# Kernel optimization log

Hardware: AMD Instinct MI355X
Metric: run time of the kernel (lower is better)

## Reference

```python
import jax, jax.numpy as jnp
import numpy as np

N, E, G = 200000, 800000, 8192
IN, H, D, EXTRA = 128, 4, 64, 16


def setup_inputs() -> dict:
    key = jax.random.key(0)
    ks = jax.random.split(key, 24)
    inp = {
        'feats_node': jax.random.normal(ks[0], (N, IN), jnp.float32),
        'feats_graph': jax.random.normal(ks[1], (G, EXTRA), jnp.float32),
        'src': jax.random.randint(ks[2], (E,), 0, N, jnp.int32),
        'dst': jax.random.randint(ks[3], (E,), 0, N, jnp.int32),
        'graph_ids': jnp.sort(jax.random.randint(ks[4], (N,), 0, G, jnp.int32)),
        # GAT layer 1: fc [H*D, IN], attn [H, D], bias zeros (DGL default)
        'fc1_w': 0.5 * jax.random.normal(ks[5], (H * D, IN), jnp.float32),
        'attn_l1': 0.5 * jax.random.normal(ks[6], (H, D), jnp.float32),
        'attn_r1': 0.5 * jax.random.normal(ks[7], (H, D), jnp.float32),
        'bias1': jnp.zeros((H * D,), jnp.float32),
        # GAT layer 2
        'fc2_w': 0.5 * jax.random.normal(ks[8], (H * D, H * D), jnp.float32),
        'attn_l2': 0.5 * jax.random.normal(ks[9], (H, D), jnp.float32),
        'attn_r2': 0.5 * jax.random.normal(ks[10], (H, D), jnp.float32),
        'bias2': jnp.zeros((H * D,), jnp.float32),
        # GAT layer 3: 1 head
        'fc3_w': 0.5 * jax.random.normal(ks[11], (D, H * D), jnp.float32),
        'attn_l3': 0.5 * jax.random.normal(ks[12], (1, D), jnp.float32),
        'attn_r3': 0.5 * jax.random.normal(ks[13], (1, D), jnp.float32),
        'bias3': jnp.zeros((D,), jnp.float32),
        # readout score
        'score_w': 0.5 * jax.random.normal(ks[14], (1, D), jnp.float32),
        'score_b': jnp.zeros((1,), jnp.float32),
        # MLP: [D+EXTRA -> 2D -> D -> 1]
        'mlp_w1': 0.5 * jax.random.normal(ks[15], (2 * D, D + EXTRA), jnp.float32),
        'mlp_b1': jnp.zeros((2 * D,), jnp.float32),
        'mlp_w2': 0.5 * jax.random.normal(ks[16], (D, 2 * D), jnp.float32),
        'mlp_b2': jnp.zeros((D,), jnp.float32),
        'mlp_w3': 0.5 * jax.random.normal(ks[17], (1, D), jnp.float32),
        'mlp_b3': jnp.zeros((1,), jnp.float32),
    }
    return inp


def gat_conv(x, src, dst, fc_w, attn_l, attn_r, bias, n_heads, out_dim):
    # DGL GATConv: proj -> edge leaky_relu attention -> per-dst softmax -> aggregate
    n = x.shape[0]
    feat = (x @ fc_w.T).reshape(n, n_heads, out_dim)          # [N,H,D]
    el = jnp.einsum('nhd,hd->nh', feat, attn_l)               # [N,H]
    er = jnp.einsum('nhd,hd->nh', feat, attn_r)
    e = jax.nn.leaky_relu(el[src] + er[dst], 0.2)             # [E,H]
    m = jax.ops.segment_max(e, dst, num_segments=n)           # per-dst max
    m = jax.lax.stop_gradient(jnp.where(jnp.isfinite(m), m, 0.0))
    a = jnp.exp(e - m[dst])                                   # [E,H]
    denom = jax.ops.segment_sum(a, dst, num_segments=n)       # [N,H]
    alpha = a / jnp.where(denom[dst] == 0, 1.0, denom[dst])
    out = jax.ops.segment_sum(alpha[:, :, None] * feat[src], dst, num_segments=n)
    return out + bias.reshape(1, n_heads, out_dim)            # [N,H,D]


def reference(feats_node, feats_graph, src, dst, graph_ids,
              fc1_w, attn_l1, attn_r1, bias1,
              fc2_w, attn_l2, attn_r2, bias2,
              fc3_w, attn_l3, attn_r3, bias3,
              score_w, score_b,
              mlp_w1, mlp_b1, mlp_w2, mlp_b2, mlp_w3, mlp_b3):
    n = feats_node.shape[0]
    g = feats_graph.shape[0]
    x = jax.nn.selu(gat_conv(feats_node, src, dst, fc1_w, attn_l1, attn_r1, bias1, H, D)).reshape(n, H * D)
    x = jax.nn.selu(gat_conv(x, src, dst, fc2_w, attn_l2, attn_r2, bias2, H, D)).reshape(n, H * D)
    x = jax.nn.selu(gat_conv(x, src, dst, fc3_w, attn_l3, attn_r3, bias3, 1, D)).reshape(n, D)
    # weighted-average readout: sum(w*x)/sum(w) per graph
    w = jax.nn.sigmoid(x @ score_w.T + score_b)               # [N,1]
    num = jax.ops.segment_sum(w * x, graph_ids, num_segments=g)
    den = jax.ops.segment_sum(w, graph_ids, num_segments=g)
    emb = num / jnp.where(den == 0, 1.0, den)                 # [G,D]
    z = jnp.concatenate([emb, feats_graph], axis=1)           # [G,D+EXTRA]
    h = jax.nn.selu(z @ mlp_w1.T + mlp_b1)
    h = jax.nn.selu(h @ mlp_w2.T + mlp_b2)
    return h @ mlp_w3.T + mlp_b3                              # [G,1]
```

## Files before the change

kernel.cpp:

```cpp
#include <hip/hip_runtime.h>
#include <math.h>

#define N_NODES 200000
#define N_EDGES 800000
#define N_GRAPHS 8192
#define B1 16
#define B2G 16
#define EC2 128

typedef unsigned short ushort_t;

__device__ __forceinline__ float selu_f(float x){
  const float alpha = 1.6732632423543772f;
  const float lam   = 1.0507009873554805f;
  return x > 0.f ? lam * x : lam * alpha * (expf(x) - 1.f);
}

__global__ void zero_i32(int* p, int n){
  int i = blockIdx.x * 256 + threadIdx.x;
  if (i < n) p[i] = 0;
}

__global__ void deg_kernel(const int* __restrict__ dst, int* __restrict__ deg, int E){
  int e = blockIdx.x * 256 + threadIdx.x;
  if (e < E) atomicAdd(&deg[dst[e]], 1);
}

__global__ void scan1(const int* __restrict__ deg, int* __restrict__ rp, int* __restrict__ bs, int n){
  __shared__ int sh[256];
  int t = threadIdx.x;
  int base = blockIdx.x * 1024;
  int v[4]; int s = 0;
  #pragma unroll
  for (int i = 0; i < 4; i++){
    int idx = base + t * 4 + i;
    v[i] = (idx < n) ? deg[idx] : 0;
    s += v[i];
  }
  sh[t] = s; __syncthreads();
  for (int off = 1; off < 256; off <<= 1){
    int x = (t >= off) ? sh[t - off] : 0;
    __syncthreads();
    sh[t] += x;
    __syncthreads();
  }
  int run = (t == 0) ? 0 : sh[t - 1];
  #pragma unroll
  for (int i = 0; i < 4; i++){
    int idx = base + t * 4 + i;
    if (idx < n) rp[idx] = run;
    run += v[i];
  }
  if (t == 255) bs[blockIdx.x] = sh[255];
}

__global__ void scan2(int* bs, int nb){
  __shared__ int sh[256];
  int t = threadIdx.x;
  sh[t] = (t < nb) ? bs[t] : 0; __syncthreads();
  for (int off = 1; off < 256; off <<= 1){
    int x = (t >= off) ? sh[t - off] : 0;
    __syncthreads();
    sh[t] += x;
    __syncthreads();
  }
  int excl = (t == 0) ? 0 : sh[t - 1];
  if (t < nb) bs[t] = excl;
}

__global__ void scan3(int* rp, const int* __restrict__ bs, int n, int total){
  int i = blockIdx.x * 256 + threadIdx.x;
  if (i < n) rp[i] += bs[i >> 10];
  if (i == 0) rp[n] = total;
}

__global__ void fill_csr(const int* __restrict__ src, const int* __restrict__ dst,
                         const int* __restrict__ rp, int* __restrict__ fil,
                         int* __restrict__ csr, int E){
  int e = blockIdx.x * 256 + threadIdx.x;
  if (e < E){
    int d = dst[e];
    int p = atomicAdd(&fil[d], 1);
    csr[rp[d] + p] = src[e];
  }
}

__global__ void wt_kernel(const float* __restrict__ W1, const float* __restrict__ W2,
                          float* __restrict__ W1t, float* __restrict__ W2t){
  int i = blockIdx.x * 256 + threadIdx.x;
  if (i < 32768){
    int k = i >> 8, m = i & 255;
    W1t[i] = W1[(size_t)m * 128 + k];
  } else if (i < 32768 + 65536){
    int j = i - 32768;
    int k = j >> 8, m = j & 255;
    W2t[j] = W2[(size_t)m * 256 + k];
  }
}

__global__ void compute_v(const float* __restrict__ W1, const float* __restrict__ al1, const float* __restrict__ ar1,
                          const float* __restrict__ W2, const float* __restrict__ al2, const float* __restrict__ ar2,
                          const float* __restrict__ W3, const float* __restrict__ al3, const float* __restrict__ ar3,
                          float* __restrict__ V1L, float* __restrict__ V1R,
                          float* __restrict__ V2L, float* __restrict__ V2R,
                          float* __restrict__ V3L, float* __restrict__ V3R){
  int i = blockIdx.x * 256 + threadIdx.x;
  if (i < 512){
    int h = i >> 7, k = i & 127;
    float sl = 0.f, sr = 0.f;
    for (int dd = 0; dd < 64; dd++){
      float w = W1[(size_t)(h * 64 + dd) * 128 + k];
      sl += al1[h * 64 + dd] * w;
      sr += ar1[h * 64 + dd] * w;
    }
    V1L[i] = sl; V1R[i] = sr;
  } else if (i < 1536){
    int j = i - 512;
    int h = j >> 8, k = j & 255;
    float sl = 0.f, sr = 0.f;
    for (int dd = 0; dd < 64; dd++){
      float w = W2[(size_t)(h * 64 + dd) * 256 + k];
      sl += al2[h * 64 + dd] * w;
      sr += ar2[h * 64 + dd] * w;
    }
    V2L[j] = sl; V2R[j] = sr;
  } else if (i < 1792){
    int k = i - 1536;
    float sl = 0.f, sr = 0.f;
    for (int dd = 0; dd < 64; dd++){
      float w = W3[(size_t)dd * 256 + k];
      sl += al3[dd] * w;
      sr += ar3[dd] * w;
    }
    V3L[k] = sl; V3R[k] = sr;
  }
}

__global__ __launch_bounds__(256) void el_er1(const float* __restrict__ x0,
                                              const float* __restrict__ V1L, const float* __restrict__ V1R,
                                              float* __restrict__ el1, float* __restrict__ er1, int n){
  __shared__ float vl[512], vr[512];
  int t = threadIdx.x;
  for (int i = t; i < 512; i += 256){ vl[i] = V1L[i]; vr[i] = V1R[i]; }
  __syncthreads();
  int node = blockIdx.x * 4 + (t >> 6);
  int l = t & 63;
  if (node >= n) return;
  float xa = x0[(size_t)node * 128 + l];
  float xb = x0[(size_t)node * 128 + 64 + l];
  #pragma unroll
  for (int h = 0; h < 4; h++){
    float pl = xa * vl[h * 128 + l] + xb * vl[h * 128 + 64 + l];
    float pr = xa * vr[h * 128 + l] + xb * vr[h * 128 + 64 + l];
    #pragma unroll
    for (int off = 32; off; off >>= 1){ pl += __shfl_xor(pl, off); pr += __shfl_xor(pr, off); }
    if (l == 0){ el1[(size_t)node * 4 + h] = pl; er1[(size_t)node * 4 + h] = pr; }
  }
}

__global__ __launch_bounds__(256) void alpha_h4(const float* __restrict__ el, const float* __restrict__ er,
                                                const int* __restrict__ rp, const int* __restrict__ csr,
                                                float* __restrict__ a, int n){
  int node = blockIdx.x * 256 + threadIdx.x;
  if (node >= n) return;
  int s0 = rp[node], s1 = rp[node + 1];
  if (s0 >= s1) return;
  float4 erv = *reinterpret_cast<const float4*>(er + (size_t)node * 4);
  float m0 = -1e30f, m1 = -1e30f, m2 = -1e30f, m3 = -1e30f;
  for (int i = s0; i < s1; i++){
    float4 e = *reinterpret_cast<const float4*>(el + (size_t)csr[i] * 4);
    float e0 = e.x + erv.x; e0 = e0 > 0.f ? e0 : 0.2f * e0; m0 = fmaxf(m0, e0);
    float e1 = e.y + erv.y; e1 = e1 > 0.f ? e1 : 0.2f * e1; m1 = fmaxf(m1, e1);
    float e2 = e.z + erv.z; e2 = e2 > 0.f ? e2 : 0.2f * e2; m2 = fmaxf(m2, e2);
    float e3 = e.w + erv.w; e3 = e3 > 0.f ? e3 : 0.2f * e3; m3 = fmaxf(m3, e3);
  }
  float d0 = 0.f, d1 = 0.f, d2 = 0.f, d3 = 0.f;
  for (int i = s0; i < s1; i++){
    float4 e = *reinterpret_cast<const float4*>(el + (size_t)csr[i] * 4);
    float e0 = e.x + erv.x; e0 = e0 > 0.f ? e0 : 0.2f * e0; d0 += expf(e0 - m0);
    float e1 = e.y + erv.y; e1 = e1 > 0.f ? e1 : 0.2f * e1; d1 += expf(e1 - m1);
    float e2 = e.z + erv.z; e2 = e2 > 0.f ? e2 : 0.2f * e2; d2 += expf(e2 - m2);
    float e3 = e.w + erv.w; e3 = e3 > 0.f ? e3 : 0.2f * e3; d3 += expf(e3 - m3);
  }
  d0 = 1.f / d0; d1 = 1.f / d1; d2 = 1.f / d2; d3 = 1.f / d3;
  for (int i = s0; i < s1; i++){
    float4 e = *reinterpret_cast<const float4*>(el + (size_t)csr[i] * 4);
    float4 o;
    float e0 = e.x + erv.x; e0 = e0 > 0.f ? e0 : 0.2f * e0; o.x = expf(e0 - m0) * d0;
    float e1 = e.y + erv.y; e1 = e1 > 0.f ? e1 : 0.2f * e1; o.y = expf(e1 - m1) * d1;
    float e2 = e.z + erv.z; e2 = e2 > 0.f ? e2 : 0.2f * e2; o.z = expf(e2 - m2) * d2;
    float e3 = e.w + erv.w; e3 = e3 > 0.f ? e3 : 0.2f * e3; o.w = expf(e3 - m3) * d3;
    *reinterpret_cast<float4*>(a + (size_t)i * 4) = o;
  }
}

__global__ __launch_bounds__(256) void alpha_h1(const float* __restrict__ el, const float* __restrict__ er,
                                                const int* __restrict__ rp, const int* __restrict__ csr,
                                                float* __restrict__ a, int n){
  int node = blockIdx.x * 256 + threadIdx.x;
  if (node >= n) return;
  int s0 = rp[node], s1 = rp[node + 1];
  if (s0 >= s1) return;
  float erv = er[node];
  float m = -1e30f;
  for (int i = s0; i < s1; i++){
    float e = el[csr[i]] + erv; e = e > 0.f ? e : 0.2f * e; m = fmaxf(m, e);
  }
  float den = 0.f;
  for (int i = s0; i < s1; i++){
    float e = el[csr[i]] + erv; e = e > 0.f ? e : 0.2f * e; den += expf(e - m);
  }
  float inv = 1.f / den;
  for (int i = s0; i < s1; i++){
    float e = el[csr[i]] + erv; e = e > 0.f ? e : 0.2f * e; a[i] = expf(e - m) * inv;
  }
}

__global__ __launch_bounds__(512, 4) void l1_fused(
    const float* __restrict__ x0, const float* __restrict__ W1t, const float* __restrict__ bias1,
    const float* __restrict__ a1, const float* __restrict__ W2t,
    const float* __restrict__ V2L, const float* __restrict__ V2R,
    const int* __restrict__ rp, const int* __restrict__ csr,
    ushort_t* __restrict__ y1hi, unsigned char* __restrict__ y1lo,
    float* __restrict__ el2, float* __restrict__ er2){
  __shared__ float aggT[4][B1][132];
  __shared__ int rpc[B1 + 1];
  float* x1s = &aggT[0][0][0];
  int t = threadIdx.x;
  int nb0 = blockIdx.x * B1;
  if (t <= B1) rpc[t] = rp[nb0 + t];
  __syncthreads();

  {
    int g = t >> 5, c4 = t & 31;
    int i0 = rpc[g], i1 = rpc[g + 1];
    float acc[4][4] = {{0.f}};
    for (int i = i0; i < i1; i += 4){
      float4 av[4]; float4 xv[4];
      #pragma unroll
      for (int j = 0; j < 4; j++){
        int idx = i + j;
        bool vld = idx < i1;
        int idc = vld ? idx : i1 - 1;
        int s = csr[idc];
        float4 a = *reinterpret_cast<const float4*>(a1 + (size_t)idc * 4);
        if (!vld) a = make_float4(0.f, 0.f, 0.f, 0.f);
        av[j] = a;
        xv[j] = *reinterpret_cast<const float4*>(x0 + (size_t)s * 128 + c4 * 4);
      }
      #pragma unroll
      for (int j = 0; j < 4; j++){
        acc[0][0] += av[j].x * xv[j].x; acc[0][1] += av[j].x * xv[j].y;
        acc[0][2] += av[j].x * xv[j].z; acc[0][3] += av[j].x * xv[j].w;
        acc[1][0] += av[j].y * xv[j].x; acc[1][1] += av[j].y * xv[j].y;
        acc[1][2] += av[j].y * xv[j].z; acc[1][3] += av[j].y * xv[j].w;
        acc[2][0] += av[j].z * xv[j].x; acc[2][1] += av[j].z * xv[j].y;
        acc[2][2] += av[j].z * xv[j].z; acc[2][3] += av[j].z * xv[j].w;
        acc[3][0] += av[j].w * xv[j].x; acc[3][1] += av[j].w * xv[j].y;
        acc[3][2] += av[j].w * xv[j].z; acc[3][3] += av[j].w * xv[j].w;
      }
    }
    #pragma unroll
    for (int h = 0; h < 4; h++){
      float4 v = make_float4(acc[h][0], acc[h][1], acc[h][2], acc[h][3]);
      *reinterpret_cast<float4*>(&aggT[h][g][c4 * 4]) = v;
    }
  }
  __syncthreads();

  int wv = t >> 6, ln = t & 63;
  int mq = wv * 8 + (ln & 7);
  int dg = ln >> 3;
  int m0 = mq * 4;
  int hh = mq >> 4;

  float acc1[4][2];
  {
    #pragma unroll
    for (int j = 0; j < 4; j++){ acc1[j][0] = 0.f; acc1[j][1] = 0.f; }
    #pragma unroll 2
    for (int kq = 0; kq < 32; kq++){
      int k = kq * 4;
      float4 w0 = *reinterpret_cast<const float4*>(W1t + (size_t)(k + 0) * 256 + m0);
      float4 w1 = *reinterpret_cast<const float4*>(W1t + (size_t)(k + 1) * 256 + m0);
      float4 w2 = *reinterpret_cast<const float4*>(W1t + (size_t)(k + 2) * 256 + m0);
      float4 w3 = *reinterpret_cast<const float4*>(W1t + (size_t)(k + 3) * 256 + m0);
      float4 a0 = *reinterpret_cast<const float4*>(&aggT[hh][dg][k]);
      float4 a1v = *reinterpret_cast<const float4*>(&aggT[hh][dg + 8][k]);
      acc1[0][0] += w0.x * a0.x + w1.x * a0.y + w2.x * a0.z + w3.x * a0.w;
      acc1[1][0] += w0.y * a0.x + w1.y * a0.y + w2.y * a0.z + w3.y * a0.w;
      acc1[2][0] += w0.z * a0.x + w1.z * a0.y + w2.z * a0.z + w3.z * a0.w;
      acc1[3][0] += w0.w * a0.x + w1.w * a0.y + w2.w * a0.z + w3.w * a0.w;
      acc1[0][1] += w0.x * a1v.x + w1.x * a1v.y + w2.x * a1v.z + w3.x * a1v.w;
      acc1[1][1] += w0.y * a1v.x + w1.y * a1v.y + w2.y * a1v.z + w3.y * a1v.w;
      acc1[2][1] += w0.z * a1v.x + w1.z * a1v.y + w2.z * a1v.z + w3.z * a1v.w;
      acc1[3][1] += w0.w * a1v.x + w1.w * a1v.y + w2.w * a1v.z + w3.w * a1v.w;
    }
  }
  __syncthreads();
  {
    float4 b = *reinterpret_cast<const float4*>(bias1 + m0);
    #pragma unroll
    for (int r = 0; r < 2; r++){
      int d = dg + 8 * r;
      float4 v;
      v.x = selu_f(acc1[0][r] + b.x);
      v.y = selu_f(acc1[1][r] + b.y);
      v.z = selu_f(acc1[2][r] + b.z);
      v.w = selu_f(acc1[3][r] + b.w);
      *reinterpret_cast<float4*>(&x1s[d * 260 + m0]) = v;
    }
  }
  __syncthreads();

  {
    float acc2[4][2];
    #pragma unroll
    for (int j = 0; j < 4; j++){ acc2[j][0] = 0.f; acc2[j][1] = 0.f; }
    #pragma unroll 2
    for (int kq = 0; kq < 64; kq++){
      int k = kq * 4;
      float4 w0 = *reinterpret_cast<const float4*>(W2t + (size_t)(k + 0) * 256 + m0);
      float4 w1 = *reinterpret_cast<const float4*>(W2t + (size_t)(k + 1) * 256 + m0);
      float4 w2 = *reinterpret_cast<const float4*>(W2t + (size_t)(k + 2) * 256 + m0);
      float4 w3 = *reinterpret_cast<const float4*>(W2t + (size_t)(k + 3) * 256 + m0);
      float4 x0v = *reinterpret_cast<const float4*>(&x1s[dg * 260 + k]);
      float4 x1v = *reinterpret_cast<const float4*>(&x1s[(dg + 8) * 260 + k]);
      acc2[0][0] += w0.x * x0v.x + w1.x * x0v.y + w2.x * x0v.z + w3.x * x0v.w;
      acc2[1][0] += w0.y * x0v.x + w1.y * x0v.y + w2.y * x0v.z + w3.y * x0v.w;
      acc2[2][0] += w0.z * x0v.x + w1.z * x0v.y + w2.z * x0v.z + w3.z * x0v.w;
      acc2[3][0] += w0.w * x0v.x + w1.w * x0v.y + w2.w * x0v.z + w3.w * x0v.w;
      acc2[0][1] += w0.x * x1v.x + w1.x * x1v.y + w2.x * x1v.z + w3.x * x1v.w;
      acc2[1][1] += w0.y * x1v.x + w1.y * x1v.y + w2.y * x1v.z + w3.y * x1v.w;
      acc2[2][1] += w0.z * x1v.x + w1.z * x1v.y + w2.z * x1v.z + w3.z * x1v.w;
      acc2[3][1] += w0.w * x1v.x + w1.w * x1v.y + w2.w * x1v.z + w3.w * x1v.w;
    }
    #pragma unroll
    for (int r = 0; r < 2; r++){
      int d = dg + 8 * r;
      unsigned int u0 = __float_as_uint(acc2[0][r]) + 0x80u;
      unsigned int u1 = __float_as_uint(acc2[1][r]) + 0x80u;
      unsigned int u2 = __float_as_uint(acc2[2][r]) + 0x80u;
      unsigned int u3 = __float_as_uint(acc2[3][r]) + 0x80u;
      ushort4 h4; uchar4 l4;
      h4.x = (ushort_t)(u0 >> 16); h4.y = (ushort_t)(u1 >> 16);
      h4.z = (ushort_t)(u2 >> 16); h4.w = (ushort_t)(u3 >> 16);
      l4.x = (unsigned char)(u0 >> 8); l4.y = (unsigned char)(u1 >> 8);
      l4.z = (unsigned char)(u2 >> 8); l4.w = (unsigned char)(u3 >> 8);
      size_t base = (size_t)(nb0 + d) * 256 + m0;
      *reinterpret_cast<ushort4*>(y1hi + base) = h4;
      *reinterpret_cast<uchar4*>(y1lo + base) = l4;
    }
  }

  if (t < 128){
    int d = t & 15, hq = (t >> 4) & 3, lr = t >> 6;
    const float* V = lr ? V2R : V2L;
    const float4* Vq = reinterpret_cast<const float4*>(V + hq * 256);
    const float4* Xq = reinterpret_cast<const float4*>(&x1s[d * 260]);
    float p = 0.f;
    #pragma unroll 4
    for (int q = 0; q < 64; q++){
      float4 v = Vq[q]; float4 x = Xq[q];
      p += v.x * x.x; p += v.y * x.y; p += v.z * x.z; p += v.w * x.w;
    }
    if (lr) er2[(size_t)(nb0 + d) * 4 + hq] = p;
    else    el2[(size_t)(nb0 + d) * 4 + hq] = p;
  }
}

__global__ __launch_bounds__(256, 4) void l2_gather(
    const ushort_t* __restrict__ y1hi, const unsigned char* __restrict__ y1lo,
    const float* __restrict__ bias2, const float* __restrict__ a2,
    const float* __restrict__ W3,
    const float* __restrict__ V3L, const float* __restrict__ V3R,
    const int* __restrict__ rp, const int* __restrict__ csr,
    float* __restrict__ feat3, float* __restrict__ el3, float* __restrict__ er3){
  __shared__ float x2s[B2G][257];
  __shared__ float W3c[16 * 257];
  __shared__ float als[EC2][4];
  __shared__ int   ssrc[EC2];
  __shared__ int   rpc[B2G + 1];
  int t = threadIdx.x;
  int nb0 = blockIdx.x * B2G;
  if (t <= B2G) rpc[t] = rp[nb0 + t];
  __syncthreads();
  int e0 = rpc[0], eN = rpc[B2G];
  int c = t;
  int h = c >> 6;

  float acc[B2G];
  #pragma unroll
  for (int d = 0; d < B2G; d++) acc[d] = 0.f;

  for (int c0 = e0; c0 < eN; c0 += EC2){
    int ce = min(EC2, eN - c0);
    for (int i = t; i < ce; i += 256){
      ssrc[i] = csr[c0 + i];
      float4 av = *reinterpret_cast<const float4*>(a2 + (size_t)(c0 + i) * 4);
      als[i][0] = av.x; als[i][1] = av.y; als[i][2] = av.z; als[i][3] = av.w;
    }
    __syncthreads();
    #pragma unroll
    for (int d = 0; d < B2G; d++){
      int lo = max(rpc[d], c0) - c0;
      int hi = min(rpc[d + 1], c0 + ce) - c0;
      for (int i = lo; i < hi; i += 4){
        float aj[4]; unsigned int uj[4];
        #pragma unroll
        for (int j = 0; j < 4; j++){
          int idx = i + j;
          bool vld = idx < hi;
          int idc = vld ? idx : hi - 1;
          int s = ssrc[idc];
          aj[j] = vld ? als[idc][h] : 0.f;
          size_t o = (size_t)s * 256 + c;
          uj[j] = ((unsigned int)y1hi[o] << 16) | ((unsigned int)y1lo[o] << 8);
        }
        acc[d] += aj[0] * __uint_as_float(uj[0]) + aj[1] * __uint_as_float(uj[1])
                + aj[2] * __uint_as_float(uj[2]) + aj[3] * __uint_as_float(uj[3]);
      }
    }
    __syncthreads();
  }
  {
    float b = bias2[c];
    #pragma unroll
    for (int d = 0; d < B2G; d++) x2s[d][c] = selu_f(acc[d] + b);
  }
  __syncthreads();

  {
    int task = t >> 3, j = t & 7;
    int d = task & 15, lr = task >> 4;
    const float* V = lr ? V3R : V3L;
    float p = 0.f;
    for (int kk = 0; kk < 32; kk++){
      int k = j + kk * 8;
      p += V[k] * x2s[d][k];
    }
    p += __shfl_xor(p, 1); p += __shfl_xor(p, 2); p += __shfl_xor(p, 4);
    if (j == 0){ if (lr) er3[nb0 + d] = p; else el3[nb0 + d] = p; }
  }

  for (int ch = 0; ch < 4; ch++){
    __syncthreads();
    for (int i = t; i < 16 * 64; i += 256){
      int r = i >> 6, k4 = i & 63;
      float4 w = *reinterpret_cast<const float4*>(W3 + (size_t)(ch * 16 + r) * 256 + k4 * 4);
      W3c[r * 257 + k4 * 4 + 0] = w.x; W3c[r * 257 + k4 * 4 + 1] = w.y;
      W3c[r * 257 + k4 * 4 + 2] = w.z; W3c[r * 257 + k4 * 4 + 3] = w.w;
    }
    __syncthreads();
    {
      int r = t & 15, d = t >> 4;
      float s = 0.f;
      #pragma unroll 4
      for (int k = 0; k < 256; k++) s += W3c[r * 257 + k] * x2s[d][k];
      feat3[(size_t)(nb0 + d) * 64 + ch * 16 + r] = s;
    }
  }
}

__global__ __launch_bounds__(256) void gat_agg3(const float* __restrict__ feat, const float* __restrict__ a3,
                                                const int* __restrict__ rp, const int* __restrict__ csr,
                                                const float* __restrict__ bias,
                                                float* __restrict__ out, int n){
  int node = blockIdx.x * 4 + (threadIdx.x >> 6);
  int t = threadIdx.x & 63;
  if (node >= n) return;
  int s0 = rp[node], s1 = rp[node + 1];
  float acc = 0.f;
  for (int i = s0; i < s1; i += 4){
    float a[4], f[4];
    #pragma unroll
    for (int j = 0; j < 4; j++){
      int idx = i + j;
      bool vld = idx < s1;
      int idc = vld ? idx : s1 - 1;
      float av = a3[idc];
      if (!vld) av = 0.f;
      a[j] = av;
      f[j] = feat[(size_t)csr[idc] * 64 + t];
    }
    acc += a[0] * f[0] + a[1] * f[1] + a[2] * f[2] + a[3] * f[3];
  }
  out[(size_t)node * 64 + t] = selu_f(acc + bias[t]);
}

__global__ void readout_kernel(const float* __restrict__ x3, const float* __restrict__ score_w,
                               const float* __restrict__ score_b, const int* __restrict__ gids,
                               float* __restrict__ num, float* __restrict__ den, int n){
  int node = blockIdx.x * 4 + (threadIdx.x >> 6);
  int lane = threadIdx.x & 63;
  if (node >= n) return;
  float xv = x3[(size_t)node * 64 + lane];
  float p = xv * score_w[lane];
  #pragma unroll
  for (int off = 32; off; off >>= 1) p += __shfl_xor(p, off);
  float w = 1.f / (1.f + expf(-(p + score_b[0])));
  int g = gids[node];
  atomicAdd(&num[(size_t)g * 64 + lane], w * xv);
  if (lane == 0) atomicAdd(&den[g], w);
}

__global__ __launch_bounds__(128) void mlp_kernel(
    const float* __restrict__ num, const float* __restrict__ den,
    const float* __restrict__ fg,
    const float* __restrict__ w1, const float* __restrict__ b1,
    const float* __restrict__ w2, const float* __restrict__ b2,
    const float* __restrict__ w3, const float* __restrict__ b3,
    float* __restrict__ out, int G){
  __shared__ float z[80];
  __shared__ float h1[128];
  __shared__ float h2[64];
  int t = threadIdx.x;
  for (int g = blockIdx.x; g < G; g += gridDim.x){
    if (t < 64){
      float d = den[g];
      d = (d == 0.f) ? 1.f : d;
      z[t] = num[(size_t)g * 64 + t] / d;
    } else if (t < 80){
      z[t] = fg[(size_t)g * 16 + (t - 64)];
    }
    __syncthreads();
    {
      float a = b1[t];
      for (int k = 0; k < 80; k++) a += z[k] * w1[t * 80 + k];
      h1[t] = selu_f(a);
    }
    __syncthreads();
    if (t < 64){
      float a = b2[t];
      for (int k = 0; k < 128; k++) a += h1[k] * w2[t * 128 + k];
      h2[t] = selu_f(a);
    }
    __syncthreads();
    if (t < 64){
      float p = h2[t] * w3[t];
      #pragma unroll
      for (int off = 32; off; off >>= 1) p += __shfl_down(p, off);
      if (t == 0) out[g] = p + b3[0];
    }
    __syncthreads();
  }
}

extern "C" void kernel_launch(void* const* d_in, const int* in_sizes, int n_in,
                              void* d_out, int out_size, void* d_ws, size_t ws_size,
                              hipStream_t stream) {
  const float* feats_node  = (const float*)d_in[0];
  const float* feats_graph = (const float*)d_in[1];
  const int*   src         = (const int*)d_in[2];
  const int*   dst         = (const int*)d_in[3];
  const int*   gids        = (const int*)d_in[4];
  const float* fc1_w   = (const float*)d_in[5];
  const float* attn_l1 = (const float*)d_in[6];
  const float* attn_r1 = (const float*)d_in[7];
  const float* bias1   = (const float*)d_in[8];
  const float* fc2_w   = (const float*)d_in[9];
  const float* attn_l2 = (const float*)d_in[10];
  const float* attn_r2 = (const float*)d_in[11];
  const float* bias2   = (const float*)d_in[12];
  const float* fc3_w   = (const float*)d_in[13];
  const float* attn_l3 = (const float*)d_in[14];
  const float* attn_r3 = (const float*)d_in[15];
  const float* bias3   = (const float*)d_in[16];
  const float* score_w = (const float*)d_in[17];
  const float* score_b = (const float*)d_in[18];
  const float* mlp_w1  = (const float*)d_in[19];
  const float* mlp_b1  = (const float*)d_in[20];
  const float* mlp_w2  = (const float*)d_in[21];
  const float* mlp_b2  = (const float*)d_in[22];
  const float* mlp_w3  = (const float*)d_in[23];
  const float* mlp_b3  = (const float*)d_in[24];
  float* out = (float*)d_out;

  char* ws = (char*)d_ws;
  size_t off = 0;
  auto alloc = [&](size_t bytes) -> void* {
    void* p = ws + off;
    off += (bytes + 255) / 256 * 256;
    return p;
  };
  int*   deg   = (int*)alloc((size_t)N_NODES * 4);
  int*   fil   = (int*)alloc((size_t)N_NODES * 4);
  int*   rp    = (int*)alloc((size_t)(N_NODES + 1) * 4);
  int*   bs    = (int*)alloc(256 * 4);
  int*   csr   = (int*)alloc((size_t)N_EDGES * 4);
  float* elbuf = (float*)alloc((size_t)N_NODES * 4 * 4);
  float* erbuf = (float*)alloc((size_t)N_NODES * 4 * 4);
  float* V1L   = (float*)alloc(512 * 4);
  float* V1R   = (float*)alloc(512 * 4);
  float* V2L   = (float*)alloc(1024 * 4);
  float* V2R   = (float*)alloc(1024 * 4);
  float* V3L   = (float*)alloc(256 * 4);
  float* V3R   = (float*)alloc(256 * 4);
  float* W1t   = (float*)alloc(32768 * 4);
  float* W2t   = (float*)alloc(65536 * 4);
  float* num   = (float*)alloc((size_t)N_GRAPHS * 64 * 4);
  float* den   = (float*)alloc((size_t)N_GRAPHS * 4);
  float* A     = (float*)alloc((size_t)N_EDGES * 4 * 4);
  float* feat3 = (float*)alloc((size_t)N_NODES * 64 * 4);
  ushort_t*      y1hi = (ushort_t*)alloc((size_t)N_NODES * 256 * 2);
  unsigned char* y1lo = (unsigned char*)alloc((size_t)N_NODES * 256);
  float* x3 = (float*)y1hi;

  zero_i32<<<(N_NODES + 255) / 256, 256, 0, stream>>>(deg, N_NODES);
  zero_i32<<<(N_NODES + 255) / 256, 256, 0, stream>>>(fil, N_NODES);
  zero_i32<<<(N_GRAPHS * 64 + 255) / 256, 256, 0, stream>>>((int*)num, N_GRAPHS * 64);
  zero_i32<<<(N_GRAPHS + 255) / 256, 256, 0, stream>>>((int*)den, N_GRAPHS);

  deg_kernel<<<(N_EDGES + 255) / 256, 256, 0, stream>>>(dst, deg, N_EDGES);
  scan1<<<196, 256, 0, stream>>>(deg, rp, bs, N_NODES);
  scan2<<<1, 256, 0, stream>>>(bs, 196);
  scan3<<<(N_NODES + 255) / 256, 256, 0, stream>>>(rp, bs, N_NODES, N_EDGES);
  fill_csr<<<(N_EDGES + 255) / 256, 256, 0, stream>>>(src, dst, rp, fil, csr, N_EDGES);

  compute_v<<<7, 256, 0, stream>>>(fc1_w, attn_l1, attn_r1, fc2_w, attn_l2, attn_r2,
                                   fc3_w, attn_l3, attn_r3, V1L, V1R, V2L, V2R, V3L, V3R);
  wt_kernel<<<384, 256, 0, stream>>>(fc1_w, fc2_w, W1t, W2t);
  el_er1<<<N_NODES / 4, 256, 0, stream>>>(feats_node, V1L, V1R, elbuf, erbuf, N_NODES);

  alpha_h4<<<(N_NODES + 255) / 256, 256, 0, stream>>>(elbuf, erbuf, rp, csr, A, N_NODES);
  l1_fused<<<N_NODES / B1, 512, 0, stream>>>(feats_node, W1t, bias1, A, W2t,
                                             V2L, V2R, rp, csr, y1hi, y1lo, elbuf, erbuf);
  alpha_h4<<<(N_NODES + 255) / 256, 256, 0, stream>>>(elbuf, erbuf, rp, csr, A, N_NODES);
  l2_gather<<<N_NODES / B2G, 256, 0, stream>>>(y1hi, y1lo, bias2, A, fc3_w,
                                               V3L, V3R, rp, csr, feat3, elbuf, erbuf);
  alpha_h1<<<(N_NODES + 255) / 256, 256, 0, stream>>>(elbuf, erbuf, rp, csr, A, N_NODES);
  gat_agg3<<<N_NODES / 4, 256, 0, stream>>>(feat3, A, rp, csr, bias3, x3, N_NODES);

  readout_kernel<<<N_NODES / 4, 256, 0, stream>>>(x3, score_w, score_b, gids, num, den, N_NODES);
  mlp_kernel<<<256, 128, 0, stream>>>(num, den, feats_graph,
                                      mlp_w1, mlp_b1, mlp_w2, mlp_b2, mlp_w3, mlp_b3,
                                      out, N_GRAPHS);
}
```

Before: 2.274 ms.

## Sort nodes by in-degree to balance per-block gather work in GAT layers

Builds a permutation of nodes bucketed by in-degree (histogram, prefix and scatter) and makes l1_fused, l2_gather and gat_agg3 process nodes in that order, so each block's nodes have similar degree and lanes diverge less. l2_gather also drops its shared-memory edge-chunk staging and its syncs, and reads csr and alpha directly from global memory per destination. The cost is three extra small kernels, atomics on 64 bins, and output writes scattered through the permutation instead of contiguous, which hurts coalescing and locality. Bucketing of nodes within a bin is nondeterministic because it uses atomics.

```diff
diff --git a/kernel.cpp b/kernel.cpp
--- a/kernel.cpp
+++ b/kernel.cpp
@@ -6,7 +6,6 @@
 #define N_GRAPHS 8192
 #define B1 16
 #define B2G 16
-#define EC2 128
 
 typedef unsigned short ushort_t;
 
@@ -82,6 +81,34 @@
     int d = dst[e];
     int p = atomicAdd(&fil[d], 1);
     csr[rp[d] + p] = src[e];
+  }
+}
+
+__global__ void hist_kernel(const int* __restrict__ deg, int* __restrict__ hist, int n){
+  int i = blockIdx.x * 256 + threadIdx.x;
+  if (i < n) atomicAdd(&hist[min(deg[i], 63)], 1);
+}
+
+__global__ void prefix64(const int* __restrict__ hist, int* __restrict__ boff){
+  __shared__ int sh[64];
+  int t = threadIdx.x;
+  sh[t] = hist[t]; __syncthreads();
+  for (int off = 1; off < 64; off <<= 1){
+    int x = (t >= off) ? sh[t - off] : 0;
+    __syncthreads();
+    sh[t] += x;
+    __syncthreads();
+  }
+  boff[t] = (t == 0) ? 0 : sh[t - 1];
+}
+
+__global__ void scatter_perm(const int* __restrict__ deg, int* __restrict__ boff,
+                             int* __restrict__ perm, int n){
+  int i = blockIdx.x * 256 + threadIdx.x;
+  if (i < n){
+    int b = min(deg[i], 63);
+    int p = atomicAdd(&boff[b], 1);
+    perm[p] = i;
   }
 }
 
@@ -220,20 +247,25 @@
     const float* __restrict__ x0, const float* __restrict__ W1t, const float* __restrict__ bias1,
     const float* __restrict__ a1, const float* __restrict__ W2t,
     const float* __restrict__ V2L, const float* __restrict__ V2R,
-    const int* __restrict__ rp, const int* __restrict__ csr,
+    const int* __restrict__ rp, const int* __restrict__ csr, const int* __restrict__ perm,
     ushort_t* __restrict__ y1hi, unsigned char* __restrict__ y1lo,
     float* __restrict__ el2, float* __restrict__ er2){
   __shared__ float aggT[4][B1][132];
-  __shared__ int rpc[B1 + 1];
+  __shared__ int pnode[B1], rps[B1], rpe[B1];
   float* x1s = &aggT[0][0][0];
   int t = threadIdx.x;
   int nb0 = blockIdx.x * B1;
-  if (t <= B1) rpc[t] = rp[nb0 + t];
+  if (t < B1){
+    int nd = perm[nb0 + t];
+    pnode[t] = nd;
+    rps[t] = rp[nd];
+    rpe[t] = rp[nd + 1];
+  }
   __syncthreads();
 
   {
     int g = t >> 5, c4 = t & 31;
-    int i0 = rpc[g], i1 = rpc[g + 1];
+    int i0 = rps[g], i1 = rpe[g];
     float acc[4][4] = {{0.f}};
     for (int i = i0; i < i1; i += 4){
       float4 av[4]; float4 xv[4];
@@ -347,7 +379,7 @@
       h4.z = (ushort_t)(u2 >> 16); h4.w = (ushort_t)(u3 >> 16);
       l4.x = (unsigned char)(u0 >> 8); l4.y = (unsigned char)(u1 >> 8);
       l4.z = (unsigned char)(u2 >> 8); l4.w = (unsigned char)(u3 >> 8);
-      size_t base = (size_t)(nb0 + d) * 256 + m0;
+      size_t base = (size_t)pnode[d] * 256 + m0;
       *reinterpret_cast<ushort4*>(y1hi + base) = h4;
       *reinterpret_cast<uchar4*>(y1lo + base) = l4;
     }
@@ -364,8 +396,8 @@
       float4 v = Vq[q]; float4 x = Xq[q];
       p += v.x * x.x; p += v.y * x.y; p += v.z * x.z; p += v.w * x.w;
     }
-    if (lr) er2[(size_t)(nb0 + d) * 4 + hq] = p;
-    else    el2[(size_t)(nb0 + d) * 4 + hq] = p;
+    if (lr) er2[(size_t)pnode[d] * 4 + hq] = p;
+    else    el2[(size_t)pnode[d] * 4 + hq] = p;
   }
 }
 
@@ -374,18 +406,20 @@
     const float* __restrict__ bias2, const float* __restrict__ a2,
     const float* __restrict__ W3,
     const float* __restrict__ V3L, const float* __restrict__ V3R,
-    const int* __restrict__ rp, const int* __restrict__ csr,
+    const int* __restrict__ rp, const int* __restrict__ csr, const int* __restrict__ perm,
     float* __restrict__ feat3, float* __restrict__ el3, float* __restrict__ er3){
   __shared__ float x2s[B2G][257];
   __shared__ float W3c[16 * 257];
-  __shared__ float als[EC2][4];
-  __shared__ int   ssrc[EC2];
-  __shared__ int   rpc[B2G + 1];
+  __shared__ int pnode[B2G], rps[B2G], rpe[B2G];
   int t = threadIdx.x;
   int nb0 = blockIdx.x * B2G;
-  if (t <= B2G) rpc[t] = rp[nb0 + t];
+  if (t < B2G){
+    int nd = perm[nb0 + t];
+    pnode[t] = nd;
+    rps[t] = rp[nd];
+    rpe[t] = rp[nd + 1];
+  }
   __syncthreads();
-  int e0 = rpc[0], eN = rpc[B2G];
   int c = t;
   int h = c >> 6;
 
@@ -393,35 +427,24 @@
   #pragma unroll
   for (int d = 0; d < B2G; d++) acc[d] = 0.f;
 
-  for (int c0 = e0; c0 < eN; c0 += EC2){
-    int ce = min(EC2, eN - c0);
-    for (int i = t; i < ce; i += 256){
-      ssrc[i] = csr[c0 + i];
-      float4 av = *reinterpret_cast<const float4*>(a2 + (size_t)(c0 + i) * 4);
-      als[i][0] = av.x; als[i][1] = av.y; als[i][2] = av.z; als[i][3] = av.w;
-    }
-    __syncthreads();
-    #pragma unroll
-    for (int d = 0; d < B2G; d++){
-      int lo = max(rpc[d], c0) - c0;
-      int hi = min(rpc[d + 1], c0 + ce) - c0;
-      for (int i = lo; i < hi; i += 4){
-        float aj[4]; unsigned int uj[4];
-        #pragma unroll
-        for (int j = 0; j < 4; j++){
-          int idx = i + j;
-          bool vld = idx < hi;
-          int idc = vld ? idx : hi - 1;
-          int s = ssrc[idc];
-          aj[j] = vld ? als[idc][h] : 0.f;
-          size_t o = (size_t)s * 256 + c;
-          uj[j] = ((unsigned int)y1hi[o] << 16) | ((unsigned int)y1lo[o] << 8);
-        }
-        acc[d] += aj[0] * __uint_as_float(uj[0]) + aj[1] * __uint_as_float(uj[1])
-                + aj[2] * __uint_as_float(uj[2]) + aj[3] * __uint_as_float(uj[3]);
+  #pragma unroll
+  for (int d = 0; d < B2G; d++){
+    int i0 = rps[d], i1 = rpe[d];
+    for (int i = i0; i < i1; i += 4){
+      float aj[4]; unsigned int uj[4];
+      #pragma unroll
+      for (int j = 0; j < 4; j++){
+        int idx = i + j;
+        bool vld = idx < i1;
+        int idc = vld ? idx : i1 - 1;
+        int s = csr[idc];
+        aj[j] = vld ? a2[(size_t)idc * 4 + h] : 0.f;
+        size_t o = (size_t)s * 256 + c;
+        uj[j] = ((unsigned int)y1hi[o] << 16) | ((unsigned int)y1lo[o] << 8);
       }
-    }
-    __syncthreads();
+      acc[d] += aj[0] * __uint_as_float(uj[0]) + aj[1] * __uint_as_float(uj[1])
+              + aj[2] * __uint_as_float(uj[2]) + aj[3] * __uint_as_float(uj[3]);
+    }
   }
   {
     float b = bias2[c];
@@ -440,7 +463,7 @@
       p += V[k] * x2s[d][k];
     }
     p += __shfl_xor(p, 1); p += __shfl_xor(p, 2); p += __shfl_xor(p, 4);
-    if (j == 0){ if (lr) er3[nb0 + d] = p; else el3[nb0 + d] = p; }
+    if (j == 0){ if (lr) er3[pnode[d]] = p; else el3[pnode[d]] = p; }
   }
 
   for (int ch = 0; ch < 4; ch++){
@@ -457,18 +480,20 @@
       float s = 0.f;
       #pragma unroll 4
       for (int k = 0; k < 256; k++) s += W3c[r * 257 + k] * x2s[d][k];
-      feat3[(size_t)(nb0 + d) * 64 + ch * 16 + r] = s;
+      feat3[(size_t)pnode[d] * 64 + ch * 16 + r] = s;
     }
   }
 }
 
 __global__ __launch_bounds__(256) void gat_agg3(const float* __restrict__ feat, const float* __restrict__ a3,
                                                 const int* __restrict__ rp, const int* __restrict__ csr,
+                                                const int* __restrict__ perm,
                                                 const float* __restrict__ bias,
                                                 float* __restrict__ out, int n){
-  int node = blockIdx.x * 4 + (threadIdx.x >> 6);
+  int slot = blockIdx.x * 4 + (threadIdx.x >> 6);
   int t = threadIdx.x & 63;
-  if (node >= n) return;
+  if (slot >= n) return;
+  int node = perm[slot];
   int s0 = rp[node], s1 = rp[node + 1];
   float acc = 0.f;
   for (int i = s0; i < s1; i += 4){
@@ -588,6 +613,9 @@
   int*   rp    = (int*)alloc((size_t)(N_NODES + 1) * 4);
   int*   bs    = (int*)alloc(256 * 4);
   int*   csr   = (int*)alloc((size_t)N_EDGES * 4);
+  int*   hist  = (int*)alloc(64 * 4);
+  int*   boff  = (int*)alloc(64 * 4);
+  int*   perm  = (int*)alloc((size_t)N_NODES * 4);
   float* elbuf = (float*)alloc((size_t)N_NODES * 4 * 4);
   float* erbuf = (float*)alloc((size_t)N_NODES * 4 * 4);
   float* V1L   = (float*)alloc(512 * 4);
@@ -608,6 +636,7 @@
 
   zero_i32<<<(N_NODES + 255) / 256, 256, 0, stream>>>(deg, N_NODES);
   zero_i32<<<(N_NODES + 255) / 256, 256, 0, stream>>>(fil, N_NODES);
+  zero_i32<<<1, 256, 0, stream>>>(hist, 64);
   zero_i32<<<(N_GRAPHS * 64 + 255) / 256, 256, 0, stream>>>((int*)num, N_GRAPHS * 64);
   zero_i32<<<(N_GRAPHS + 255) / 256, 256, 0, stream>>>((int*)den, N_GRAPHS);
 
@@ -617,6 +646,10 @@
   scan3<<<(N_NODES + 255) / 256, 256, 0, stream>>>(rp, bs, N_NODES, N_EDGES);
   fill_csr<<<(N_EDGES + 255) / 256, 256, 0, stream>>>(src, dst, rp, fil, csr, N_EDGES);
 
+  hist_kernel<<<(N_NODES + 255) / 256, 256, 0, stream>>>(deg, hist, N_NODES);
+  prefix64<<<1, 64, 0, stream>>>(hist, boff);
+  scatter_perm<<<(N_NODES + 255) / 256, 256, 0, stream>>>(deg, boff, perm, N_NODES);
+
   compute_v<<<7, 256, 0, stream>>>(fc1_w, attn_l1, attn_r1, fc2_w, attn_l2, attn_r2,
                                    fc3_w, attn_l3, attn_r3, V1L, V1R, V2L, V2R, V3L, V3R);
   wt_kernel<<<384, 256, 0, stream>>>(fc1_w, fc2_w, W1t, W2t);
@@ -624,12 +657,12 @@
 
   alpha_h4<<<(N_NODES + 255) / 256, 256, 0, stream>>>(elbuf, erbuf, rp, csr, A, N_NODES);
   l1_fused<<<N_NODES / B1, 512, 0, stream>>>(feats_node, W1t, bias1, A, W2t,
-                                             V2L, V2R, rp, csr, y1hi, y1lo, elbuf, erbuf);
+                                             V2L, V2R, rp, csr, perm, y1hi, y1lo, elbuf, erbuf);
   alpha_h4<<<(N_NODES + 255) / 256, 256, 0, stream>>>(elbuf, erbuf, rp, csr, A, N_NODES);
   l2_gather<<<N_NODES / B2G, 256, 0, stream>>>(y1hi, y1lo, bias2, A, fc3_w,
-                                               V3L, V3R, rp, csr, feat3, elbuf, erbuf);
+                                               V3L, V3R, rp, csr, perm, feat3, elbuf, erbuf);
   alpha_h1<<<(N_NODES + 255) / 256, 256, 0, stream>>>(elbuf, erbuf, rp, csr, A, N_NODES);
-  gat_agg3<<<N_NODES / 4, 256, 0, stream>>>(feat3, A, rp, csr, bias3, x3, N_NODES);
+  gat_agg3<<<N_NODES / 4, 256, 0, stream>>>(feat3, A, rp, csr, perm, bias3, x3, N_NODES);
 
   readout_kernel<<<N_NODES / 4, 256, 0, stream>>>(x3, score_w, score_b, gids, num, den, N_NODES);
   mlp_kernel<<<256, 128, 0, stream>>>(num, den, feats_graph,
```

Measured after the change: 4.138 ms. +82.0%, slower.
